# Optimization experiments

Measured on AMD Instinct MI355X. Metric: run time of the kernel, lower is better.

Reference implementation:

```python
import jax, jax.numpy as jnp
import numpy as np

B, H, SQ, SKV, D, TOPK = 1, 16, 1024, 4096, 128, 64


def setup_inputs() -> dict:
    key = jax.random.key(0)
    kq, kk, kv, ki, ks = jax.random.split(key, 5)
    q = jax.random.normal(kq, (B, H, SQ, D), dtype=jnp.float32)
    k = jax.random.normal(kk, (B, H, SKV, D), dtype=jnp.float32)
    v = jax.random.normal(kv, (B, H, SKV, D), dtype=jnp.float32)
    topk_indices = jax.random.randint(ki, (B, SQ, TOPK), 0, SKV, dtype=jnp.int32)
    topk_scores = jax.random.uniform(ks, (B, SQ, TOPK), dtype=jnp.float32)
    return {"q": q, "k": k, "v": v, "topk_indices": topk_indices,
            "topk_scores": topk_scores}


def reference(q, k, v, topk_indices, topk_scores):
    # q: (b,h,s,d); k,v: (b,h,S,d) global (cp_world_size=1 all-gather is identity)
    head_dim = q.shape[-1]
    scale = head_dim ** -0.5
    # Gather selected K/V per query without dense (b,h,s,S,d) expansion.
    # idx: (b,1,s,topk,1) broadcast against (b,h,1,S,d) along axis=3.
    idx = topk_indices[:, None, :, :, None]
    k_g = jnp.take_along_axis(k[:, :, None, :, :], idx, axis=3)  # (b,h,s,t,d)
    v_g = jnp.take_along_axis(v[:, :, None, :, :], idx, axis=3)  # (b,h,s,t,d)
    scores = jnp.einsum("bhsd,bhstd->bhst", q, k_g) * scale
    w = jax.nn.softmax(scores, axis=-1)
    # rescale by indexer scores and renormalize
    w = w * topk_scores[:, None, :, :]
    w = w / (jnp.sum(w, axis=-1, keepdims=True) + 1e-12)
    out = jnp.einsum("bhst,bhstd->bhsd", w, v_g)
    return out
```

## Files before the change

### kernel.cpp

```cpp
#include <hip/hip_runtime.h>
#include <hip/hip_fp16.h>

#define NH  16
#define SQL 1024
#define SKV 4096
#define HD  128
#define TK  64

typedef _Float16 h2_t __attribute__((ext_vector_type(2)));

__device__ __forceinline__ unsigned pkh(float x, float y) {
    return (unsigned)__half_as_ushort(__float2half(x)) |
           ((unsigned)__half_as_ushort(__float2half(y)) << 16);
}

__global__ __launch_bounds__(256) void cvt_f16(
    const float* __restrict__ k, const float* __restrict__ v,
    unsigned short* __restrict__ kh, unsigned short* __restrict__ vh)
{
    int b = blockIdx.x;
    const float* src; unsigned short* dst;
    if (b < 4096) { src = k; dst = kh; }
    else          { src = v; dst = vh; b -= 4096; }
    const size_t i = (size_t)b * 256 + threadIdx.x;
    const float4* s4 = (const float4*)src;
    float4 a = s4[2 * i], c = s4[2 * i + 1];
    uint4 o;
    o.x = pkh(a.x, a.y);
    o.y = pkh(a.z, a.w);
    o.z = pkh(c.x, c.y);
    o.w = pkh(c.z, c.w);
    ((uint4*)dst)[i] = o;
}

__global__ __launch_bounds__(256) void dsa_f16(
    const float* __restrict__ q, const unsigned short* __restrict__ kh,
    const unsigned short* __restrict__ vh, const int* __restrict__ tidx,
    const float* __restrict__ tsc, float* __restrict__ out)
{
    __shared__ float scr[4][TK][17];

    const int tid  = threadIdx.x;
    const int wv   = tid >> 6;
    const int lane = tid & 63;
    const int quad = lane >> 4;
    const int l16  = lane & 15;
    const int bi   = blockIdx.x;

    const int h = ((bi >> 11) << 3) | (bi & 7);
    const int s = (((bi >> 3) & 255) << 2) + wv;

    const float* qp = q + (size_t)(h * SQL + s) * HD + 8 * l16;
    const float4 qa = *(const float4*)qp;
    const float4 qb = *(const float4*)(qp + 4);
    h2_t q0 = {(_Float16)qa.x, (_Float16)qa.y};
    h2_t q1 = {(_Float16)qa.z, (_Float16)qa.w};
    h2_t q2 = {(_Float16)qb.x, (_Float16)qb.y};
    h2_t q3 = {(_Float16)qb.z, (_Float16)qb.w};

    const int   t_idx = tidx[s * TK + lane];
    const float t_sc  = tsc[s * TK + lane];

    const unsigned short* kb = kh + (size_t)h * SKV * HD;
    float part[16];
#pragma unroll
    for (int i = 0; i < 16; ++i) {
        const size_t row = (size_t)__shfl(t_idx, 4 * i + quad);
        uint4 kw = *(const uint4*)(kb + row * HD + 8 * l16);
        float d = 0.f;
#if __has_builtin(__builtin_amdgcn_fdot2)
        d = __builtin_amdgcn_fdot2(q0, __builtin_bit_cast(h2_t, kw.x), d, false);
        d = __builtin_amdgcn_fdot2(q1, __builtin_bit_cast(h2_t, kw.y), d, false);
        d = __builtin_amdgcn_fdot2(q2, __builtin_bit_cast(h2_t, kw.z), d, false);
        d = __builtin_amdgcn_fdot2(q3, __builtin_bit_cast(h2_t, kw.w), d, false);
#else
        {
            float2 k0 = __half22float2(__builtin_bit_cast(__half2, kw.x));
            float2 k1 = __half22float2(__builtin_bit_cast(__half2, kw.y));
            float2 k2 = __half22float2(__builtin_bit_cast(__half2, kw.z));
            float2 k3 = __half22float2(__builtin_bit_cast(__half2, kw.w));
            d  = qa.x * k0.x + qa.y * k0.y + qa.z * k1.x + qa.w * k1.y;
            d += qb.x * k2.x + qb.y * k2.y + qb.z * k3.x + qb.w * k3.y;
        }
#endif
        part[i] = d;
    }

    const unsigned short* vb = vh + (size_t)h * SKV * HD;
    uint4 vw[16];
#pragma unroll
    for (int i = 0; i < 16; ++i) {
        const size_t row = (size_t)__shfl(t_idx, 4 * i + quad);
        vw[i] = *(const uint4*)(vb + row * HD + 8 * l16);
    }

#pragma unroll
    for (int i = 0; i < 16; ++i) scr[wv][4 * i + quad][l16] = part[i];
    float acc = 0.f;
#pragma unroll
    for (int m = 0; m < 16; ++m) acc += scr[wv][lane][m];
    acc *= 0.08838834764831845f;

    float m = acc;
#pragma unroll
    for (int off = 32; off; off >>= 1) m = fmaxf(m, __shfl_xor(m, off));
    const float e   = __expf(acc - m);
    const float ets = e * t_sc;
    float se = e, sets = ets;
#pragma unroll
    for (int off = 32; off; off >>= 1) {
        se   += __shfl_xor(se, off);
        sets += __shfl_xor(sets, off);
    }
    const float w = ets / (sets + 1e-12f * se);
    const unsigned wpk = __builtin_bit_cast(unsigned, __float2half2_rn(w));

    __half2 o0 = __float2half2_rn(0.f);
    __half2 o1 = o0, o2 = o0, o3 = o0;
#pragma unroll
    for (int i = 0; i < 16; ++i) {
        const __half2 w2 = __builtin_bit_cast(__half2, __shfl(wpk, 4 * i + quad));
        o0 = __hfma2(w2, __builtin_bit_cast(__half2, vw[i].x), o0);
        o1 = __hfma2(w2, __builtin_bit_cast(__half2, vw[i].y), o1);
        o2 = __hfma2(w2, __builtin_bit_cast(__half2, vw[i].z), o2);
        o3 = __hfma2(w2, __builtin_bit_cast(__half2, vw[i].w), o3);
    }

    __half2 oo[4] = {o0, o1, o2, o3};
#pragma unroll
    for (int j = 0; j < 4; ++j) {
        unsigned u = __builtin_bit_cast(unsigned, oo[j]);
        oo[j] = __hadd2(oo[j], __builtin_bit_cast(__half2, __shfl_xor(u, 16)));
        u = __builtin_bit_cast(unsigned, oo[j]);
        oo[j] = __hadd2(oo[j], __builtin_bit_cast(__half2, __shfl_xor(u, 32)));
    }

    if (quad == 0) {
        float2 f0 = __half22float2(oo[0]);
        float2 f1 = __half22float2(oo[1]);
        float2 f2 = __half22float2(oo[2]);
        float2 f3 = __half22float2(oo[3]);
        float* op = out + (size_t)(h * SQL + s) * HD + 8 * l16;
        *(float4*)op       = make_float4(f0.x, f0.y, f1.x, f1.y);
        *(float4*)(op + 4) = make_float4(f2.x, f2.y, f3.x, f3.y);
    }
}

__global__ __launch_bounds__(256) void dsa_fp32(
    const float* __restrict__ q, const float* __restrict__ k,
    const float* __restrict__ v, const int* __restrict__ tidx,
    const float* __restrict__ tsc, float* __restrict__ out)
{
    __shared__ int   idxs[4][TK];
    __shared__ float wsc[4][TK];
    const int tid = threadIdx.x, wv = tid >> 6, lane = tid & 63;
    const int half = lane >> 5, l32 = lane & 31, bi = blockIdx.x;
    const int h = ((bi & 7) << 1) | ((bi >> 3) & 1);
    const int s = ((bi >> 4) << 2) + wv;
    const float* qp = q + (size_t)(h * SQL + s) * HD;
    const float4 qf = *(const float4*)(qp + 4 * l32);
    const float t_sc = tsc[s * TK + lane];
    idxs[wv][lane] = tidx[s * TK + lane];
    const float* kb = k + (size_t)h * SKV * HD;
#pragma unroll 4
    for (int i = 0; i < TK / 2; ++i) {
        const int t = 2 * i + half, row = idxs[wv][t];
        float4 k4 = *(const float4*)(kb + (size_t)row * HD + 4 * l32);
        float d = k4.x * qf.x + k4.y * qf.y + k4.z * qf.z + k4.w * qf.w;
        d += __shfl_xor(d, 16); d += __shfl_xor(d, 8); d += __shfl_xor(d, 4);
        d += __shfl_xor(d, 2);  d += __shfl_xor(d, 1);
        if (l32 == 0) wsc[wv][t] = d;
    }
    float acc = wsc[wv][lane] * 0.08838834764831845f;
    float m = acc;
#pragma unroll
    for (int off = 32; off; off >>= 1) m = fmaxf(m, __shfl_xor(m, off));
    const float e = __expf(acc - m), ets = e * t_sc;
    float se = e, sets = ets;
#pragma unroll
    for (int off = 32; off; off >>= 1) { se += __shfl_xor(se, off); sets += __shfl_xor(sets, off); }
    wsc[wv][lane] = ets / (sets + 1e-12f * se);
    const float* vbp = v + (size_t)h * SKV * HD;
    float4 o = make_float4(0.f, 0.f, 0.f, 0.f);
#pragma unroll 4
    for (int i = 0; i < TK / 2; ++i) {
        const int t = 2 * i + half, row = idxs[wv][t];
        const float wt = wsc[wv][t];
        float4 v4 = *(const float4*)(vbp + (size_t)row * HD + 4 * l32);
        o.x += wt * v4.x; o.y += wt * v4.y; o.z += wt * v4.z; o.w += wt * v4.w;
    }
    o.x += __shfl_xor(o.x, 32); o.y += __shfl_xor(o.y, 32);
    o.z += __shfl_xor(o.z, 32); o.w += __shfl_xor(o.w, 32);
    if (half == 0) *(float4*)(out + (size_t)(h * SQL + s) * HD + 4 * l32) = o;
}

extern "C" void kernel_launch(void* const* d_in, const int* in_sizes, int n_in,
                              void* d_out, int out_size, void* d_ws, size_t ws_size,
                              hipStream_t stream) {
    const float* q  = (const float*)d_in[0];
    const float* k  = (const float*)d_in[1];
    const float* v  = (const float*)d_in[2];
    const int*   ti = (const int*)d_in[3];
    const float* ts = (const float*)d_in[4];
    float* out = (float*)d_out;

    const size_t nkv  = (size_t)NH * SKV * HD;
    const size_t need = 2 * nkv * sizeof(unsigned short);
    if (ws_size >= need) {
        unsigned short* kh = (unsigned short*)d_ws;
        unsigned short* vh = kh + nkv;
        cvt_f16<<<dim3(8192), dim3(256), 0, stream>>>(k, v, kh, vh);
        dsa_f16<<<dim3(4096), dim3(256), 0, stream>>>(q, kh, vh, ti, ts, out);
    } else {
        dsa_fp32<<<dim3(4096), dim3(256), 0, stream>>>(q, k, v, ti, ts, out);
    }
}
```

Before: 133.9 us.

## Process multiple queries and heads per wave in a phased persistent-style kernel

The attention kernel now launches far fewer blocks, each wave handling 4 queries across 2 heads of the same XCD. Indices and scores are loaded once and reused across the two heads, and K scoring runs for all queries before a separate V accumulation phase. Q loads and output stores become nontemporal, and launch bounds request 2 blocks per CU. The cost is less parallelism (512 blocks), more serial work per wave, and V loads that are no longer prefetched ahead of the softmax.

```diff
diff --git a/kernel.cpp b/kernel.cpp
--- a/kernel.cpp
+++ b/kernel.cpp
@@ -8,6 +8,7 @@
 #define TK  64
 
 typedef _Float16 h2_t __attribute__((ext_vector_type(2)));
+typedef float    f32x4 __attribute__((ext_vector_type(4)));
 
 __device__ __forceinline__ unsigned pkh(float x, float y) {
     return (unsigned)__half_as_ushort(__float2half(x)) |
@@ -33,7 +34,7 @@
     ((uint4*)dst)[i] = o;
 }
 
-__global__ __launch_bounds__(256) void dsa_f16(
+__global__ __launch_bounds__(256, 2) void dsa_phased(
     const float* __restrict__ q, const unsigned short* __restrict__ kh,
     const unsigned short* __restrict__ vh, const int* __restrict__ tidx,
     const float* __restrict__ tsc, float* __restrict__ out)
@@ -46,103 +47,122 @@
     const int quad = lane >> 4;
     const int l16  = lane & 15;
     const int bi   = blockIdx.x;
-
-    const int h = ((bi >> 11) << 3) | (bi & 7);
-    const int s = (((bi >> 3) & 255) << 2) + wv;
-
-    const float* qp = q + (size_t)(h * SQL + s) * HD + 8 * l16;
-    const float4 qa = *(const float4*)qp;
-    const float4 qb = *(const float4*)(qp + 4);
-    h2_t q0 = {(_Float16)qa.x, (_Float16)qa.y};
-    h2_t q1 = {(_Float16)qa.z, (_Float16)qa.w};
-    h2_t q2 = {(_Float16)qb.x, (_Float16)qb.y};
-    h2_t q3 = {(_Float16)qb.z, (_Float16)qb.w};
-
-    const int   t_idx = tidx[s * TK + lane];
-    const float t_sc  = tsc[s * TK + lane];
-
-    const unsigned short* kb = kh + (size_t)h * SKV * HD;
-    float part[16];
-#pragma unroll
-    for (int i = 0; i < 16; ++i) {
-        const size_t row = (size_t)__shfl(t_idx, 4 * i + quad);
-        uint4 kw = *(const uint4*)(kb + row * HD + 8 * l16);
-        float d = 0.f;
+    const int xcd  = bi & 7;
+    const int tile = bi >> 3;
+    const int sb   = tile * 16 + wv * 4;
+
+    int   tIdx[4];
+    float tSc[4];
+#pragma unroll
+    for (int qi = 0; qi < 4; ++qi) {
+        tIdx[qi] = tidx[(sb + qi) * TK + lane];
+        tSc[qi]  = tsc[(sb + qi) * TK + lane];
+    }
+
+    for (int rnd = 0; rnd < 2; ++rnd) {
+        const int h = xcd | (rnd << 3);
+        const unsigned short* kb = kh + (size_t)h * SKV * HD;
+        const unsigned short* vb = vh + (size_t)h * SKV * HD;
+        unsigned wpk[4];
+
+#pragma unroll
+        for (int qi = 0; qi < 4; ++qi) {
+            const int s = sb + qi;
+            const float* qp = q + (size_t)(h * SQL + s) * HD + 8 * l16;
+            const f32x4 qa = __builtin_nontemporal_load((const f32x4*)qp);
+            const f32x4 qb = __builtin_nontemporal_load((const f32x4*)qp + 1);
+            h2_t q0 = {(_Float16)qa.x, (_Float16)qa.y};
+            h2_t q1 = {(_Float16)qa.z, (_Float16)qa.w};
+            h2_t q2 = {(_Float16)qb.x, (_Float16)qb.y};
+            h2_t q3 = {(_Float16)qb.z, (_Float16)qb.w};
+
+            float part[16];
+#pragma unroll
+            for (int i = 0; i < 16; ++i) {
+                const size_t row = (size_t)__shfl(tIdx[qi], 4 * i + quad);
+                uint4 kw = *(const uint4*)(kb + row * HD + 8 * l16);
+                float d = 0.f;
 #if __has_builtin(__builtin_amdgcn_fdot2)
-        d = __builtin_amdgcn_fdot2(q0, __builtin_bit_cast(h2_t, kw.x), d, false);
-        d = __builtin_amdgcn_fdot2(q1, __builtin_bit_cast(h2_t, kw.y), d, false);
-        d = __builtin_amdgcn_fdot2(q2, __builtin_bit_cast(h2_t, kw.z), d, false);
-        d = __builtin_amdgcn_fdot2(q3, __builtin_bit_cast(h2_t, kw.w), d, false);
+                d = __builtin_amdgcn_fdot2(q0, __builtin_bit_cast(h2_t, kw.x), d, false);
+                d = __builtin_amdgcn_fdot2(q1, __builtin_bit_cast(h2_t, kw.y), d, false);
+                d = __builtin_amdgcn_fdot2(q2, __builtin_bit_cast(h2_t, kw.z), d, false);
+                d = __builtin_amdgcn_fdot2(q3, __builtin_bit_cast(h2_t, kw.w), d, false);
 #else
-        {
-            float2 k0 = __half22float2(__builtin_bit_cast(__half2, kw.x));
-            float2 k1 = __half22float2(__builtin_bit_cast(__half2, kw.y));
-            float2 k2 = __half22float2(__builtin_bit_cast(__half2, kw.z));
-            float2 k3 = __half22float2(__builtin_bit_cast(__half2, kw.w));
-            d  = qa.x * k0.x + qa.y * k0.y + qa.z * k1.x + qa.w * k1.y;
-            d += qb.x * k2.x + qb.y * k2.y + qb.z * k3.x + qb.w * k3.y;
+                {
+                    float2 k0 = __half22float2(__builtin_bit_cast(__half2, kw.x));
+                    float2 k1 = __half22float2(__builtin_bit_cast(__half2, kw.y));
+                    float2 k2 = __half22float2(__builtin_bit_cast(__half2, kw.z));
+                    float2 k3 = __half22float2(__builtin_bit_cast(__half2, kw.w));
+                    d  = qa.x * k0.x + qa.y * k0.y + qa.z * k1.x + qa.w * k1.y;
+                    d += qb.x * k2.x + qb.y * k2.y + qb.z * k3.x + qb.w * k3.y;
+                }
+#endif
+                part[i] = d;
+            }
+
+#pragma unroll
+            for (int i = 0; i < 16; ++i) scr[wv][4 * i + quad][l16] = part[i];
+            float acc = 0.f;
+#pragma unroll
+            for (int m = 0; m < 16; ++m) acc += scr[wv][lane][m];
+            acc *= 0.08838834764831845f;
+
+            float mx = acc;
+#pragma unroll
+            for (int off = 32; off; off >>= 1) mx = fmaxf(mx, __shfl_xor(mx, off));
+            const float e   = __expf(acc - mx);
+            const float ets = e * tSc[qi];
+            float se = e, sets = ets;
+#pragma unroll
+            for (int off = 32; off; off >>= 1) {
+                se   += __shfl_xor(se, off);
+                sets += __shfl_xor(sets, off);
+            }
+            const float w = ets / (sets + 1e-12f * se);
+            wpk[qi] = __builtin_bit_cast(unsigned, __float2half2_rn(w));
         }
-#endif
-        part[i] = d;
-    }
-
-    const unsigned short* vb = vh + (size_t)h * SKV * HD;
-    uint4 vw[16];
-#pragma unroll
-    for (int i = 0; i < 16; ++i) {
-        const size_t row = (size_t)__shfl(t_idx, 4 * i + quad);
-        vw[i] = *(const uint4*)(vb + row * HD + 8 * l16);
-    }
-
-#pragma unroll
-    for (int i = 0; i < 16; ++i) scr[wv][4 * i + quad][l16] = part[i];
-    float acc = 0.f;
-#pragma unroll
-    for (int m = 0; m < 16; ++m) acc += scr[wv][lane][m];
-    acc *= 0.08838834764831845f;
-
-    float m = acc;
-#pragma unroll
-    for (int off = 32; off; off >>= 1) m = fmaxf(m, __shfl_xor(m, off));
-    const float e   = __expf(acc - m);
-    const float ets = e * t_sc;
-    float se = e, sets = ets;
-#pragma unroll
-    for (int off = 32; off; off >>= 1) {
-        se   += __shfl_xor(se, off);
-        sets += __shfl_xor(sets, off);
-    }
-    const float w = ets / (sets + 1e-12f * se);
-    const unsigned wpk = __builtin_bit_cast(unsigned, __float2half2_rn(w));
-
-    __half2 o0 = __float2half2_rn(0.f);
-    __half2 o1 = o0, o2 = o0, o3 = o0;
-#pragma unroll
-    for (int i = 0; i < 16; ++i) {
-        const __half2 w2 = __builtin_bit_cast(__half2, __shfl(wpk, 4 * i + quad));
-        o0 = __hfma2(w2, __builtin_bit_cast(__half2, vw[i].x), o0);
-        o1 = __hfma2(w2, __builtin_bit_cast(__half2, vw[i].y), o1);
-        o2 = __hfma2(w2, __builtin_bit_cast(__half2, vw[i].z), o2);
-        o3 = __hfma2(w2, __builtin_bit_cast(__half2, vw[i].w), o3);
-    }
-
-    __half2 oo[4] = {o0, o1, o2, o3};
-#pragma unroll
-    for (int j = 0; j < 4; ++j) {
-        unsigned u = __builtin_bit_cast(unsigned, oo[j]);
-        oo[j] = __hadd2(oo[j], __builtin_bit_cast(__half2, __shfl_xor(u, 16)));
-        u = __builtin_bit_cast(unsigned, oo[j]);
-        oo[j] = __hadd2(oo[j], __builtin_bit_cast(__half2, __shfl_xor(u, 32)));
-    }
-
-    if (quad == 0) {
-        float2 f0 = __half22float2(oo[0]);
-        float2 f1 = __half22float2(oo[1]);
-        float2 f2 = __half22float2(oo[2]);
-        float2 f3 = __half22float2(oo[3]);
-        float* op = out + (size_t)(h * SQL + s) * HD + 8 * l16;
-        *(float4*)op       = make_float4(f0.x, f0.y, f1.x, f1.y);
-        *(float4*)(op + 4) = make_float4(f2.x, f2.y, f3.x, f3.y);
+
+        __syncthreads();
+
+#pragma unroll
+        for (int qi = 0; qi < 4; ++qi) {
+            const int s = sb + qi;
+            __half2 o0 = __float2half2_rn(0.f);
+            __half2 o1 = o0, o2 = o0, o3 = o0;
+#pragma unroll
+            for (int i = 0; i < 16; ++i) {
+                const size_t row = (size_t)__shfl(tIdx[qi], 4 * i + quad);
+                uint4 vw = *(const uint4*)(vb + row * HD + 8 * l16);
+                const __half2 w2 =
+                    __builtin_bit_cast(__half2, __shfl(wpk[qi], 4 * i + quad));
+                o0 = __hfma2(w2, __builtin_bit_cast(__half2, vw.x), o0);
+                o1 = __hfma2(w2, __builtin_bit_cast(__half2, vw.y), o1);
+                o2 = __hfma2(w2, __builtin_bit_cast(__half2, vw.z), o2);
+                o3 = __hfma2(w2, __builtin_bit_cast(__half2, vw.w), o3);
+            }
+
+            __half2 oo[4] = {o0, o1, o2, o3};
+#pragma unroll
+            for (int j = 0; j < 4; ++j) {
+                unsigned u = __builtin_bit_cast(unsigned, oo[j]);
+                oo[j] = __hadd2(oo[j], __builtin_bit_cast(__half2, __shfl_xor(u, 16)));
+                u = __builtin_bit_cast(unsigned, oo[j]);
+                oo[j] = __hadd2(oo[j], __builtin_bit_cast(__half2, __shfl_xor(u, 32)));
+            }
+
+            if (quad == 0) {
+                float2 f0 = __half22float2(oo[0]);
+                float2 f1 = __half22float2(oo[1]);
+                float2 f2 = __half22float2(oo[2]);
+                float2 f3 = __half22float2(oo[3]);
+                float* op = out + (size_t)(h * SQL + s) * HD + 8 * l16;
+                f32x4 w0 = {f0.x, f0.y, f1.x, f1.y};
+                f32x4 w1 = {f2.x, f2.y, f3.x, f3.y};
+                __builtin_nontemporal_store(w0, (f32x4*)op);
+                __builtin_nontemporal_store(w1, (f32x4*)op + 1);
+            }
+        }
+        if (rnd == 0) __syncthreads();
     }
 }
 
@@ -210,7 +230,7 @@
         unsigned short* kh = (unsigned short*)d_ws;
         unsigned short* vh = kh + nkv;
         cvt_f16<<<dim3(8192), dim3(256), 0, stream>>>(k, v, kh, vh);
-        dsa_f16<<<dim3(4096), dim3(256), 0, stream>>>(q, kh, vh, ti, ts, out);
+        dsa_phased<<<dim3(512), dim3(256), 0, stream>>>(q, kh, vh, ti, ts, out);
     } else {
         dsa_fp32<<<dim3(4096), dim3(256), 0, stream>>>(q, k, v, ti, ts, out);
     }
```

Measured after the change: 133.5 us. About the same (-0.3%).
